# Performance work log

Hardware: AMD Instinct MI355X
Metric: run time of the kernel (lower is better)

## Reference

```python
import jax, jax.numpy as jnp
import numpy as np

N = 4096
IN_DIM = 128
OUT_DIM = 64
LEAKY_SLOPE = 0.2


def setup_inputs() -> dict:
    key = jax.random.key(0)
    ks = jax.random.split(key, 8)
    H = jax.random.normal(ks[0], (N, IN_DIM), dtype=jnp.float32)
    # dense 0/1 adjacency per relation (int constants w.r.t. autodiff)
    A_buys = jax.random.randint(ks[1], (N, N), 0, 2, dtype=jnp.int32)
    A_views = jax.random.randint(ks[2], (N, N), 0, 2, dtype=jnp.int32)
    # xavier_uniform for W (stored [in, out]; Wh = H @ W == torch Linear with weight W.T)
    s_w = float(np.sqrt(6.0 / (IN_DIM + OUT_DIM)))
    W_buys = jax.random.uniform(ks[3], (IN_DIM, OUT_DIM), jnp.float32, -s_w, s_w)
    W_views = jax.random.uniform(ks[4], (IN_DIM, OUT_DIM), jnp.float32, -s_w, s_w)
    # xavier_uniform on a.view(1, 2*out_dim)
    s_a = float(np.sqrt(6.0 / (1 + 2 * OUT_DIM)))
    a_buys = jax.random.uniform(ks[5], (2 * OUT_DIM,), jnp.float32, -s_a, s_a)
    a_views = jax.random.uniform(ks[6], (2 * OUT_DIM,), jnp.float32, -s_a, s_a)
    bias = jnp.zeros((OUT_DIM,), dtype=jnp.float32)
    return {"H": H, "A_buys": A_buys, "A_views": A_views,
            "W_buys": W_buys, "W_views": W_views,
            "a_buys": a_buys, "a_views": a_views, "bias": bias}


def _relation(H, A, W, a):
    Wh = H @ W                                  # [N, OUT]
    # (cat(Wh_i, Wh_j) * a).sum(-1) == Wh_i @ a[:OUT] + Wh_j @ a[OUT:]
    s_i = Wh @ a[:OUT_DIM]                      # [N]
    s_j = Wh @ a[OUT_DIM:]                      # [N]
    e = jax.nn.leaky_relu(s_i[:, None] + s_j[None, :], LEAKY_SLOPE)  # [N, N]
    e = jnp.where(A == 0, -jnp.inf, e)
    alpha = jnp.nan_to_num(jax.nn.softmax(e, axis=1))                # isolated rows -> 0
    return alpha @ Wh                           # [N, OUT]


def reference(H, A_buys, A_views, W_buys, W_views, a_buys, a_views, bias):
    agg = _relation(H, A_buys, W_buys, a_buys) + _relation(H, A_views, W_views, a_views)
    return agg + bias
```

## Files before the change

kernel.cpp:

```cpp
#include <hip/hip_runtime.h>

#define NN 4096
#define IND 128
#define OUTD 64
#define WJ 128
#define NWIN 8
#define LOG2E 1.44269504088896340736f

typedef __attribute__((ext_vector_type(4))) float  floatx4;
typedef __attribute__((ext_vector_type(8))) __bf16 bf16x8;
typedef __attribute__((ext_vector_type(4))) int    intx4;

#if __has_builtin(__builtin_amdgcn_exp2f)
#define EXP2(x) __builtin_amdgcn_exp2f(x)
#else
#define EXP2(x) exp2f(x)
#endif

__device__ __forceinline__ unsigned short f2bf(float f) {
  unsigned int u = __float_as_uint(f);
  u += 0x7fffu + ((u >> 16) & 1u);
  return (unsigned short)(u >> 16);
}

__global__ __launch_bounds__(256) void gat_prep(
    const float* __restrict__ H,
    const float* __restrict__ W0, const float* __restrict__ W1,
    const float* __restrict__ av0, const float* __restrict__ av1,
    unsigned short* __restrict__ whF,
    float* __restrict__ sA, float* __restrict__ sB)
{
  const int rel = blockIdx.y;
  const float* __restrict__ W  = rel ? W1 : W0;
  const float* __restrict__ av = rel ? av1 : av0;
  const int i0 = blockIdx.x * 16;
  const int t = threadIdx.x;
  const int c = t & 63;
  const int wv = __builtin_amdgcn_readfirstlane(t >> 6);
  const float* __restrict__ hp = H + (size_t)(i0 + wv * 4) * IND;

  float acc0 = 0.f, acc1 = 0.f, acc2 = 0.f, acc3 = 0.f;
#pragma unroll 8
  for (int k = 0; k < IND; k += 4) {
    float4 h0 = *(const float4*)(hp + k);
    float4 h1 = *(const float4*)(hp + IND + k);
    float4 h2 = *(const float4*)(hp + 2 * IND + k);
    float4 h3 = *(const float4*)(hp + 3 * IND + k);
    float w0 = W[(k + 0) * OUTD + c];
    float w1 = W[(k + 1) * OUTD + c];
    float w2 = W[(k + 2) * OUTD + c];
    float w3 = W[(k + 3) * OUTD + c];
    acc0 += h0.x * w0 + h0.y * w1 + h0.z * w2 + h0.w * w3;
    acc1 += h1.x * w0 + h1.y * w1 + h1.z * w2 + h1.w * w3;
    acc2 += h2.x * w0 + h2.y * w1 + h2.z * w2 + h2.w * w3;
    acc3 += h3.x * w0 + h3.y * w1 + h3.z * w2 + h3.w * w3;
  }

  const float alo = av[c] * LOG2E, ahi = av[OUTD + c] * LOG2E;
  float pa0 = acc0 * alo, pa1 = acc1 * alo, pa2 = acc2 * alo, pa3 = acc3 * alo;
  float pb0 = acc0 * ahi, pb1 = acc1 * ahi, pb2 = acc2 * ahi, pb3 = acc3 * ahi;
#pragma unroll
  for (int off = 32; off >= 1; off >>= 1) {
    pa0 += __shfl_xor(pa0, off); pa1 += __shfl_xor(pa1, off);
    pa2 += __shfl_xor(pa2, off); pa3 += __shfl_xor(pa3, off);
    pb0 += __shfl_xor(pb0, off); pb1 += __shfl_xor(pb1, off);
    pb2 += __shfl_xor(pb2, off); pb3 += __shfl_xor(pb3, off);
  }
  const int ibase = i0 + wv * 4;
  if (c == 0) {
    float* sa = sA + rel * NN + ibase;
    float* sb = sB + rel * NN + ibase;
    sa[0] = pa0; sa[1] = pa1; sa[2] = pa2; sa[3] = pa3;
    sb[0] = pb0; sb[1] = pb1; sb[2] = pb2; sb[3] = pb3;
  }

  unsigned long long packed =
      (unsigned long long)f2bf(acc0)        | ((unsigned long long)f2bf(acc1) << 16) |
      ((unsigned long long)f2bf(acc2) << 32) | ((unsigned long long)f2bf(acc3) << 48);
  *(unsigned long long*)(whF + ((size_t)(rel * 512 + (ibase >> 3)) * 64 + c) * 8 + (ibase & 7)) = packed;
}

__global__ __launch_bounds__(512, 2) void gat_fused(
    const int* __restrict__ A0, const int* __restrict__ A1,
    const unsigned short* __restrict__ whF,
    const float* __restrict__ sA, const float* __restrict__ sB,
    const float* __restrict__ bias,
    float* __restrict__ out)
{
  __shared__ char lds[8][2][4096];
  const int i0   = blockIdx.x * 16;
  const int t    = threadIdx.x;
  const int w    = t >> 6;
  const int rel  = w >> 2;
  const int lane = t & 63;
  const int quad = lane >> 4;
  const int m    = lane & 15;
  const int lj   = lane & 31;
  const int half = lane >> 5;
  const int s_st = lj >> 1;
  const int wboff = s_st * 256 + (lj & 1) * 8;
  const int* __restrict__ A = rel ? A1 : A0;
  const unsigned short* __restrict__ wh = whF + (size_t)rel * 512 * 64 * 8;
  const float* __restrict__ sbp = sB + rel * NN;

  float si_r[8];
#pragma unroll
  for (int p = 0; p < 8; p++) si_r[p] = sA[rel * NN + i0 + 2 * p + half];

  const int jbase = (w & 3) * (NWIN * WJ);

  floatx4 acc0 = {0.f,0.f,0.f,0.f}, acc1 = acc0, acc2 = acc0, acc3 = acc0, acc4 = acc0;
  bf16x8 vone;
#pragma unroll
  for (int k = 0; k < 8; k++) vone[k] = (__bf16)1.0f;

  intx4  av2[2][8];
  float4 sjv2[2];
  bf16x8 b[4][4];

  auto issueA = [&](int win) {
    const int jw = jbase + win * WJ;
    const int buf = win & 1;
    sjv2[buf] = *(const float4*)(sbp + jw + lj * 4);
    const int* pA = A + (size_t)(i0 + half) * NN + jw + lj * 4;
#pragma unroll
    for (int p = 0; p < 8; p++)
      av2[buf][p] = *(const intx4*)(pA + (size_t)(2 * p) * NN);
  };

  auto stage = [&](int win) {
    const int buf = win & 1;
    char* slice = lds[w][buf];
    const float4 sjv = sjv2[buf];
#pragma unroll
    for (int p = 0; p < 8; p++) {
      const int rp = 2 * p + half;
      const float si = si_r[p];
      float t0 = si + sjv.x, t1 = si + sjv.y, t2 = si + sjv.z, t3 = si + sjv.w;
      float e0 = EXP2(fmaxf(t0, 0.2f * t0));
      float e1 = EXP2(fmaxf(t1, 0.2f * t1));
      float e2 = EXP2(fmaxf(t2, 0.2f * t2));
      float e3 = EXP2(fmaxf(t3, 0.2f * t3));
      const intx4 a4 = av2[buf][p];
      e0 = a4[0] ? e0 : 0.f;
      e1 = a4[1] ? e1 : 0.f;
      e2 = a4[2] ? e2 : 0.f;
      e3 = a4[3] ? e3 : 0.f;
      uint2 pk;
      pk.x = (unsigned)f2bf(e0) | ((unsigned)f2bf(e1) << 16);
      pk.y = (unsigned)f2bf(e2) | ((unsigned)f2bf(e3) << 16);
      *(uint2*)(slice + wboff + ((rp ^ s_st) & 15) * 16) = pk;
    }
  };

  auto issueB = [&](int win) {
    const int jw = jbase + win * WJ;
    const unsigned short* bb = wh + ((size_t)(jw >> 3) + quad) * 512 + (size_t)m * 8;
#pragma unroll
    for (int ks = 0; ks < 4; ks++)
#pragma unroll
      for (int nt = 0; nt < 4; nt++)
        b[ks][nt] = *(const bf16x8*)(bb + (size_t)ks * 2048 + nt * 128);
  };

  auto domfma = [&](int win) {
    char* slice = lds[w][win & 1];
    bf16x8 afr[4];
#pragma unroll
    for (int ks = 0; ks < 4; ks++) {
      const int s = ks * 4 + quad;
      afr[ks] = *(const bf16x8*)(slice + s * 256 + ((m ^ s) & 15) * 16);
    }
#pragma unroll
    for (int ks = 0; ks < 4; ks++) {
      acc0 = __builtin_amdgcn_mfma_f32_16x16x32_bf16(afr[ks], b[ks][0], acc0, 0, 0, 0);
      acc1 = __builtin_amdgcn_mfma_f32_16x16x32_bf16(afr[ks], b[ks][1], acc1, 0, 0, 0);
      acc2 = __builtin_amdgcn_mfma_f32_16x16x32_bf16(afr[ks], b[ks][2], acc2, 0, 0, 0);
      acc3 = __builtin_amdgcn_mfma_f32_16x16x32_bf16(afr[ks], b[ks][3], acc3, 0, 0, 0);
      acc4 = __builtin_amdgcn_mfma_f32_16x16x32_bf16(afr[ks], vone,     acc4, 0, 0, 0);
    }
  };

  issueA(0);
  stage(0);
  issueA(1);

#pragma unroll
  for (int win = 0; win < NWIN; win++) {
    issueB(win);
    if (win + 2 < NWIN) issueA(win + 2);
    if (win + 1 < NWIN) stage(win + 1);
    domfma(win);
  }

  float* redw  = (float*)lds[w][0];
  float* dredw = (float*)lds[w][1];
#pragma unroll
  for (int r = 0; r < 4; r++) {
    const int row = quad * 4 + r;
    redw[row * 64 + 0 * 16 + m] = acc0[r];
    redw[row * 64 + 1 * 16 + m] = acc1[r];
    redw[row * 64 + 2 * 16 + m] = acc2[r];
    redw[row * 64 + 3 * 16 + m] = acc3[r];
  }
  if (m == 0) {
#pragma unroll
    for (int r = 0; r < 4; r++) dredw[quad * 4 + r] = acc4[r];
  }
  __syncthreads();

  const int c  = t & 63;
  const int r0 = t >> 6;
  const float bc = bias[c];
#pragma unroll
  for (int rr = r0; rr < 16; rr += 8) {
    float n0 = 0.f, n1 = 0.f, d0 = 0.f, d1 = 0.f;
#pragma unroll
    for (int ww = 0; ww < 4; ww++) {
      n0 += ((const float*)lds[ww][0])[rr * 64 + c];
      d0 += ((const float*)lds[ww][1])[rr];
      n1 += ((const float*)lds[ww + 4][0])[rr * 64 + c];
      d1 += ((const float*)lds[ww + 4][1])[rr];
    }
    const float inv0 = d0 > 0.f ? 1.f / d0 : 0.f;
    const float inv1 = d1 > 0.f ? 1.f / d1 : 0.f;
    out[(size_t)(i0 + rr) * OUTD + c] = n0 * inv0 + n1 * inv1 + bc;
  }
}

extern "C" void kernel_launch(void* const* d_in, const int* in_sizes, int n_in,
                              void* d_out, int out_size, void* d_ws, size_t ws_size,
                              hipStream_t stream) {
  const float* H    = (const float*)d_in[0];
  const int*   A0   = (const int*)d_in[1];
  const int*   A1   = (const int*)d_in[2];
  const float* W0   = (const float*)d_in[3];
  const float* W1   = (const float*)d_in[4];
  const float* av0  = (const float*)d_in[5];
  const float* av1  = (const float*)d_in[6];
  const float* bias = (const float*)d_in[7];
  float* out = (float*)d_out;

  const size_t whF_b = (size_t)2 * 512 * 64 * 8 * 2;
  const size_t s_b   = (size_t)2 * NN * 4;

  unsigned short* whF = (unsigned short*)d_ws;
  float*          sA  = (float*)((char*)d_ws + whF_b);
  float*          sB  = (float*)((char*)d_ws + whF_b + s_b);

  gat_prep<<<dim3(NN / 16, 2), 256, 0, stream>>>(H, W0, W1, av0, av1, whF, sA, sB);
  gat_fused<<<NN / 16, 512, 0, stream>>>(A0, A1, whF, sA, sB, bias, out);
}
```

Baseline: 184.1 us.

## Precompute adjacency bitmasks in prep kernel and read packed bits in fused kernel

The prep kernel gains extra blocks that stream both int32 adjacency matrices and pack each row into 4-bit nibbles laid out to match the fused kernel's window and lane mapping. The fused kernel then loads eight 32-bit words per lane once, instead of double-buffering large int4 adjacency loads per window. This removes register pressure and global load latency from the attention loop. In exchange, the full adjacency read moves into a separate pass with an extra workspace write and read.

```diff
diff --git a/kernel.cpp b/kernel.cpp
--- a/kernel.cpp
+++ b/kernel.cpp
@@ -25,16 +25,46 @@
 
 __global__ __launch_bounds__(256) void gat_prep(
     const float* __restrict__ H,
+    const int* __restrict__ A0, const int* __restrict__ A1,
     const float* __restrict__ W0, const float* __restrict__ W1,
     const float* __restrict__ av0, const float* __restrict__ av1,
     unsigned short* __restrict__ whF,
-    float* __restrict__ sA, float* __restrict__ sB)
+    float* __restrict__ sA, float* __restrict__ sB,
+    unsigned* __restrict__ PW)
 {
   const int rel = blockIdx.y;
+  const int t = threadIdx.x;
+
+  if (blockIdx.x >= 256) {
+    const int cb = blockIdx.x - 256;
+    const int* __restrict__ Ar = rel ? A1 : A0;
+    unsigned* __restrict__ pwr = PW + (size_t)rel * NN * 128;
+    __shared__ unsigned char nib[2][4][256];
+    for (int rr = 0; rr < 2; rr++) {
+      const int row = cb * 2 + rr;
+      const int* __restrict__ ap = Ar + (size_t)row * NN;
+#pragma unroll
+      for (int it = 0; it < 4; it++) {
+        intx4 a = *(const intx4*)(ap + it * 1024 + t * 4);
+        nib[rr][it][t] = (unsigned char)((a[0] != 0) | ((a[1] != 0) << 1) |
+                                         ((a[2] != 0) << 2) | ((a[3] != 0) << 3));
+      }
+      __syncthreads();
+      if (t < 128) {
+        const int wq = t >> 5, lj = t & 31;
+        unsigned wd = 0;
+#pragma unroll
+        for (int v = 0; v < 8; v++)
+          wd |= (unsigned)nib[rr][wq][v * 32 + lj] << (4 * v);
+        pwr[(size_t)row * 128 + t] = wd;
+      }
+    }
+    return;
+  }
+
   const float* __restrict__ W  = rel ? W1 : W0;
   const float* __restrict__ av = rel ? av1 : av0;
   const int i0 = blockIdx.x * 16;
-  const int t = threadIdx.x;
   const int c = t & 63;
   const int wv = __builtin_amdgcn_readfirstlane(t >> 6);
   const float* __restrict__ hp = H + (size_t)(i0 + wv * 4) * IND;
@@ -81,7 +111,7 @@
 }
 
 __global__ __launch_bounds__(512, 2) void gat_fused(
-    const int* __restrict__ A0, const int* __restrict__ A1,
+    const unsigned* __restrict__ PW,
     const unsigned short* __restrict__ whF,
     const float* __restrict__ sA, const float* __restrict__ sB,
     const float* __restrict__ bias,
@@ -99,7 +129,6 @@
   const int half = lane >> 5;
   const int s_st = lj >> 1;
   const int wboff = s_st * 256 + (lj & 1) * 8;
-  const int* __restrict__ A = rel ? A1 : A0;
   const unsigned short* __restrict__ wh = whF + (size_t)rel * 512 * 64 * 8;
   const float* __restrict__ sbp = sB + rel * NN;
 
@@ -107,6 +136,12 @@
 #pragma unroll
   for (int p = 0; p < 8; p++) si_r[p] = sA[rel * NN + i0 + 2 * p + half];
 
+  unsigned pw[8];
+  const unsigned* __restrict__ pwp =
+      PW + ((size_t)(rel * NN + i0 + half) * 4 + (w & 3)) * 32 + lj;
+#pragma unroll
+  for (int p = 0; p < 8; p++) pw[p] = pwp[(size_t)(2 * p) * 128];
+
   const int jbase = (w & 3) * (NWIN * WJ);
 
   floatx4 acc0 = {0.f,0.f,0.f,0.f}, acc1 = acc0, acc2 = acc0, acc3 = acc0, acc4 = acc0;
@@ -114,38 +149,30 @@
 #pragma unroll
   for (int k = 0; k < 8; k++) vone[k] = (__bf16)1.0f;
 
-  intx4  av2[2][8];
   float4 sjv2[2];
   bf16x8 b[4][4];
 
-  auto issueA = [&](int win) {
-    const int jw = jbase + win * WJ;
-    const int buf = win & 1;
-    sjv2[buf] = *(const float4*)(sbp + jw + lj * 4);
-    const int* pA = A + (size_t)(i0 + half) * NN + jw + lj * 4;
-#pragma unroll
-    for (int p = 0; p < 8; p++)
-      av2[buf][p] = *(const intx4*)(pA + (size_t)(2 * p) * NN);
+  auto issueS = [&](int win) {
+    sjv2[win & 1] = *(const float4*)(sbp + jbase + win * WJ + lj * 4);
   };
 
   auto stage = [&](int win) {
-    const int buf = win & 1;
-    char* slice = lds[w][buf];
-    const float4 sjv = sjv2[buf];
+    char* slice = lds[w][win & 1];
+    const float4 sjv = sjv2[win & 1];
 #pragma unroll
     for (int p = 0; p < 8; p++) {
       const int rp = 2 * p + half;
       const float si = si_r[p];
+      const unsigned nb = (pw[p] >> (win * 4)) & 0xFu;
       float t0 = si + sjv.x, t1 = si + sjv.y, t2 = si + sjv.z, t3 = si + sjv.w;
       float e0 = EXP2(fmaxf(t0, 0.2f * t0));
       float e1 = EXP2(fmaxf(t1, 0.2f * t1));
       float e2 = EXP2(fmaxf(t2, 0.2f * t2));
       float e3 = EXP2(fmaxf(t3, 0.2f * t3));
-      const intx4 a4 = av2[buf][p];
-      e0 = a4[0] ? e0 : 0.f;
-      e1 = a4[1] ? e1 : 0.f;
-      e2 = a4[2] ? e2 : 0.f;
-      e3 = a4[3] ? e3 : 0.f;
+      e0 = (nb & 1u) ? e0 : 0.f;
+      e1 = (nb & 2u) ? e1 : 0.f;
+      e2 = (nb & 4u) ? e2 : 0.f;
+      e3 = (nb & 8u) ? e3 : 0.f;
       uint2 pk;
       pk.x = (unsigned)f2bf(e0) | ((unsigned)f2bf(e1) << 16);
       pk.y = (unsigned)f2bf(e2) | ((unsigned)f2bf(e3) << 16);
@@ -181,14 +208,13 @@
     }
   };
 
-  issueA(0);
+  issueS(0); issueS(1);
   stage(0);
-  issueA(1);
 
 #pragma unroll
   for (int win = 0; win < NWIN; win++) {
     issueB(win);
-    if (win + 2 < NWIN) issueA(win + 2);
+    if (win + 2 < NWIN) issueS(win + 2);
     if (win + 1 < NWIN) stage(win + 1);
     domfma(win);
   }
@@ -247,7 +273,9 @@
   unsigned short* whF = (unsigned short*)d_ws;
   float*          sA  = (float*)((char*)d_ws + whF_b);
   float*          sB  = (float*)((char*)d_ws + whF_b + s_b);
-
-  gat_prep<<<dim3(NN / 16, 2), 256, 0, stream>>>(H, W0, W1, av0, av1, whF, sA, sB);
-  gat_fused<<<NN / 16, 512, 0, stream>>>(A0, A1, whF, sA, sB, bias, out);
-}
+  unsigned*       PW  = (unsigned*)((char*)d_ws + whF_b + 2 * s_b);
+
+  gat_prep<<<dim3(256 + 2048, 2), 256, 0, stream>>>(H, A0, A1, W0, W1, av0, av1,
+                                                    whF, sA, sB, PW);
+  gat_fused<<<NN / 16, 512, 0, stream>>>(PW, whF, sA, sB, bias, out);
+}
```

Result: no change. 184.3 us (+0.1%).
